# Kernel optimization log

Measured on AMD Instinct MI355X. Metric: run time of the kernel, lower is better.

The kernel has to match this reference:

```python
import jax, jax.numpy as jnp
import numpy as np

WS = 7      # window size
SHIFT = 3   # shift size
NH = 6      # num heads
C = 192     # channels
HH = 56
WW = 56
B = 32


def _rel_coords():
    ch, cw = np.meshgrid(np.arange(WS), np.arange(WS), indexing='ij')
    coords = np.stack([ch, cw]).reshape(2, -1)            # (2, 49)
    rel = coords[:, :, None] - coords[:, None, :]          # (2, 49, 49)
    rel[0] += WS - 1
    rel[1] += WS - 1
    rel[0] *= 2 * WS - 1
    return rel.sum(0)                                      # (49, 49)


def _swin_attn_mask(Hp, Wp):
    img = np.zeros((Hp, Wp), np.int32)
    cnt = 0
    for hs in (slice(0, -WS), slice(-WS, -SHIFT), slice(-SHIFT, None)):
        for ws_ in (slice(0, -WS), slice(-WS, -SHIFT), slice(-SHIFT, None)):
            img[hs, ws_] = cnt
            cnt += 1
    win = img.reshape(Hp // WS, WS, Wp // WS, WS).transpose(0, 2, 1, 3).reshape(-1, WS * WS)
    return win[:, :, None] != win[:, None, :]              # (Nw, 49, 49) bool


def setup_inputs() -> dict:
    key = jax.random.key(0)
    ks = jax.random.split(key, 8)
    s = 0.02
    return {
        'x': jax.random.normal(ks[0], (B, HH * WW, C), jnp.float32),
        'H': HH,
        'W': WW,
        'attn_mask': jnp.asarray(_swin_attn_mask(HH, WW)),
        'relative_coords': jnp.asarray(_rel_coords(), jnp.int32),
        'norm1_w': jnp.ones((C,), jnp.float32),
        'norm1_b': jnp.zeros((C,), jnp.float32),
        'qkv_w': jax.random.normal(ks[1], (3 * C, C), jnp.float32) * s,
        'rel_bias': jax.random.normal(ks[2], ((2 * WS - 1) ** 2, NH), jnp.float32) * 0.2,
        'proj_w': jax.random.normal(ks[3], (C, C), jnp.float32) * s,
        'proj_b': jnp.zeros((C,), jnp.float32),
        'norm2_w': jnp.ones((C,), jnp.float32),
        'norm2_b': jnp.zeros((C,), jnp.float32),
        'fc1_w': jax.random.normal(ks[4], (4 * C, C), jnp.float32) * s,
        'fc1_b': jnp.zeros((4 * C,), jnp.float32),
        'fc2_w': jax.random.normal(ks[5], (C, 4 * C), jnp.float32) * s,
        'fc2_b': jnp.zeros((C,), jnp.float32),
    }


def _ln(t, w, b):
    m = t.mean(-1, keepdims=True)
    v = t.var(-1, keepdims=True)
    return (t - m) / jnp.sqrt(v + 1e-5) * w + b


def reference(x, H, W, attn_mask, relative_coords, norm1_w, norm1_b, qkv_w, rel_bias,
              proj_w, proj_b, norm2_w, norm2_b, fc1_w, fc1_b, fc2_w, fc2_b):
    Bb, L, Cd = x.shape
    nh, hd = NH, C // NH
    shortcut = x
    h = _ln(x, norm1_w, norm1_b).reshape(Bb, H, W, Cd)
    pad_h = (WS - H % WS) % WS
    pad_w = (WS - W % WS) % WS
    if pad_h or pad_w:
        h = jnp.pad(h, ((0, 0), (0, pad_h), (0, pad_w), (0, 0)))
    Hp, Wp = H + pad_h, W + pad_w
    if SHIFT > 0:
        h = jnp.roll(h, (-SHIFT, -SHIFT), axis=(1, 2))
    nWh, nWw = Hp // WS, Wp // WS
    Lw = WS * WS
    win = h.reshape(Bb, nWh, WS, nWw, WS, Cd).transpose(0, 1, 3, 2, 4, 5).reshape(-1, Lw, Cd)
    B_ = win.shape[0]
    qkv = (win @ qkv_w.T).reshape(B_, Lw, 3, nh, hd).transpose(2, 0, 3, 1, 4)
    q, k, v = qkv[0], qkv[1], qkv[2]
    # NOTE: source multiplies by num_dim**0.5 (faithful quirk)
    attn = jnp.einsum('bhid,bhjd->bhij', q, k) * (Cd ** 0.5)
    bias = rel_bias[relative_coords].transpose(2, 0, 1)    # (nh, Lw, Lw)
    attn = attn + bias[None]
    if SHIFT > 0:
        Nw = attn_mask.shape[0]
        attn = attn.reshape(-1, Nw, nh, Lw, Lw)
        attn = jnp.where(attn_mask[None, :, None], -100.0, attn)
        attn = attn.reshape(B_, nh, Lw, Lw)
    attn = jax.nn.softmax(attn, axis=-1)
    out = jnp.einsum('bhij,bhjd->bhid', attn, v).transpose(0, 2, 1, 3).reshape(B_, Lw, Cd)
    out = out @ proj_w.T + proj_b
    out = out.reshape(Bb, nWh, nWw, WS, WS, Cd).transpose(0, 1, 3, 2, 4, 5).reshape(Bb, Hp, Wp, Cd)
    if SHIFT > 0:
        out = jnp.roll(out, (SHIFT, SHIFT), axis=(1, 2))
    out = out[:, :H, :W].reshape(Bb, L, Cd)
    x = shortcut + out
    h2 = _ln(x, norm2_w, norm2_b)
    h2 = jax.nn.gelu(h2 @ fc1_w.T + fc1_b, approximate=False)
    # source MLP applies GELU (drop2 = act_layer()) after fc2 (faithful quirk)
    h2 = jax.nn.gelu(h2 @ fc2_w.T + fc2_b, approximate=False)
    return x + h2
```

## Files before the change

kernel.cpp:

```cpp
#include <hip/hip_runtime.h>

#define WS7    7
#define SHIFT3 3
#define NHEAD  6
#define CCH    192
#define HDIM   32
#define HH56   56
#define LTOK   (HH56*HH56)
#define NWIN   64
#define NBATCH 32
#define NWTOT  (NBATCH*NWIN)
#define LW     49
#define MTOK   (NWTOT*LW)

typedef unsigned short u16;
typedef unsigned int   u32;
typedef __bf16 b16;
typedef b16   b16x8 __attribute__((ext_vector_type(8)));
typedef u16   u16x8 __attribute__((ext_vector_type(8)));
typedef float f32x4 __attribute__((ext_vector_type(4)));

__device__ __forceinline__ float b2f(u16 u) {
    u32 x = ((u32)u) << 16;
    return __builtin_bit_cast(float, x);
}
__device__ __forceinline__ u16 f2b(float f) {
    u32 x = __builtin_bit_cast(u32, f);
    u32 r = x + 0x7FFFu + ((x >> 16) & 1u);
    return (u16)(r >> 16);
}
__device__ __forceinline__ float gelu_exact(float x) {
    return 0.5f * x * (1.0f + erff(x * 0.7071067811865475f));
}

__device__ __forceinline__ int map_token(int m, int &b) {
    int widx = m / LW, p = m - widx * LW;
    b = widx >> 6;
    int wloc = widx & 63;
    int wh = wloc >> 3, ww = wloc & 7;
    int i = p / WS7, j = p - i * WS7;
    int gh = wh * WS7 + i + SHIFT3; if (gh >= HH56) gh -= HH56;
    int gw = ww * WS7 + j + SHIFT3; if (gw >= HH56) gw -= HH56;
    return gh * HH56 + gw;
}

__global__ __launch_bounds__(1024) void probe_kernel(const u16* __restrict__ x, int* flag) {
    __shared__ int ch, cz;
    if (threadIdx.x == 0) { ch = 0; cz = 0; }
    __syncthreads();
    int i = threadIdx.x * 16;
    u16x8 a = *(const u16x8*)(x + i);
    u16x8 b = *(const u16x8*)(x + i + 8);
    int h = 0, z = 0;
    #pragma unroll
    for (int q = 0; q < 8; q++) {
        h += (((a[q] >> 7) & 0xFF) >= 0xC0) + (((b[q] >> 7) & 0xFF) >= 0xC0);
        z += (a[q] == 0) + (b[q] == 0);
    }
    #pragma unroll
    for (int off = 32; off > 0; off >>= 1) {
        h += __shfl_xor(h, off, 64);
        z += __shfl_xor(z, off, 64);
    }
    if ((threadIdx.x & 63) == 0) { atomicAdd(&ch, h); atomicAdd(&cz, z); }
    __syncthreads();
    if (threadIdx.x == 0) *flag = (ch > 250 || cz > 2048) ? 1 : 0;
}

#define CANON_TOTAL 445302
__global__ __launch_bounds__(256) void canon_all_kernel(
    const int* __restrict__ flag,
    const void* s0, const void* s1, const void* s2,  const void* s3,
    const void* s4, const void* s5, const void* s6,  const void* s7,
    const void* s8, const void* s9, const void* s10, const void* s11,
    char* __restrict__ ws)
{
    int i = blockIdx.x * 256 + threadIdx.x;
    if (i >= CANON_TOTAL) return;
    const void* srcs[12] = {s0, s1, s2, s3, s4, s5, s6, s7, s8, s9, s10, s11};
    const int cnt[12] = {110592, 36864, 147456, 147456, 192, 192, 192, 192, 192, 768, 192, 1014};
    const int off[12] = {64, 221248, 294976, 589888, 884800, 885184, 885568, 885952, 886336, 886720, 888256, 888640};
    int seg = 0, base = 0;
    while (seg < 11 && i >= base + cnt[seg]) { base += cnt[seg]; seg++; }
    int j = i - base;
    const void* sp = srcs[seg];
    u16* dp = (u16*)(ws + off[seg]);
    dp[j] = (*flag) ? f2b(((const float*)sp)[j]) : ((const u16*)sp)[j];
}

template<int GATHER>
__global__ __launch_bounds__(256) void ln_kernel(
    const void* __restrict__ src, const u16* __restrict__ w, const u16* __restrict__ bia,
    u16* __restrict__ dst, int m_base, const int* __restrict__ flag)
{
    int wave = threadIdx.x >> 6, lane = threadIdx.x & 63;
    int mloc = blockIdx.x * 4 + wave;
    size_t row;
    if (GATHER) { int b; int l = map_token(m_base + mloc, b); row = (size_t)b * LTOK + l; }
    else row = mloc;
    float v0, v1, v2;
    if (GATHER && *flag) {
        const float* xp = (const float*)src + row * CCH;
        v0 = xp[lane]; v1 = xp[lane + 64]; v2 = xp[lane + 128];
    } else {
        const u16* xp = (const u16*)src + row * CCH;
        v0 = b2f(xp[lane]); v1 = b2f(xp[lane + 64]); v2 = b2f(xp[lane + 128]);
    }
    float s = v0 + v1 + v2, sq = v0 * v0 + v1 * v1 + v2 * v2;
    for (int off = 32; off > 0; off >>= 1) {
        s  += __shfl_xor(s, off, 64);
        sq += __shfl_xor(sq, off, 64);
    }
    float mean = s * (1.f / 192.f);
    float var  = fmaxf(sq * (1.f / 192.f) - mean * mean, 0.f);
    float rstd = rsqrtf(var + 1e-5f);
    u16* op = dst + (size_t)mloc * CCH;
    op[lane]       = f2b((v0 - mean) * rstd * b2f(w[lane])       + b2f(bia[lane]));
    op[lane + 64]  = f2b((v1 - mean) * rstd * b2f(w[lane + 64])  + b2f(bia[lane + 64]));
    op[lane + 128] = f2b((v2 - mean) * rstd * b2f(w[lane + 128]) + b2f(bia[lane + 128]));
}

__device__ __forceinline__ void stage192(const u16* __restrict__ g, int ldg, u16* s, int tid) {
    #pragma unroll
    for (int it = 0; it < 7; it++) {
        int t = it * 256 + tid;
        if (t < 1600) {
            int row = t / 25, c = t - row * 25;
            int cc = (c == 24) ? 0 : c;
            const u16* src = g + (size_t)row * ldg + cc * 8;
            u16* dst = s + (size_t)(it * 256 + (tid & ~63)) * 8;
            __builtin_amdgcn_global_load_lds(
                (const __attribute__((address_space(1))) void*)src,
                (__attribute__((address_space(3))) void*)dst, 16, 0, 0);
        }
    }
}

template<int MODE>
__global__ __launch_bounds__(256) void gemm_bt_kernel(
    const u16* __restrict__ A, const u16* __restrict__ Bm, int K, int N,
    const u16* __restrict__ bias,
    u16* __restrict__ Cb,
    u16* __restrict__ X1,
    const void* __restrict__ Xin,
    void* __restrict__ Oout, size_t o_off, int m_base,
    const int* __restrict__ flag)
{
    __shared__ __align__(16) u16 As[64 * 200];
    __shared__ __align__(16) u16 Bs[64 * 200];
    int isf = *flag;
    int tid = threadIdx.x;
    int m0 = blockIdx.x * 64, n0 = blockIdx.y * 64;
    int wave = tid >> 6, lane = tid & 63;
    int wm = wave >> 1, wn = wave & 1;
    int quad = lane >> 4, mr = lane & 15;
    f32x4 acc00 = {}, acc01 = {}, acc10 = {}, acc11 = {};

    const u16* pa0 = &As[(wm * 32 + mr) * 200 + quad * 8];
    const u16* pb0 = &Bs[(wn * 32 + mr) * 200 + quad * 8];

    for (int k0 = 0; k0 < K; k0 += 192) {
        if (k0) __syncthreads();
        stage192(A  + (size_t)m0 * K + k0, K, As, tid);
        stage192(Bm + (size_t)n0 * K + k0, K, Bs, tid);
        __syncthreads();
        #pragma unroll
        for (int ks = 0; ks < 6; ks++) {
            b16x8 a0 = __builtin_bit_cast(b16x8, *(const u16x8*)(pa0 + ks * 32));
            b16x8 a1 = __builtin_bit_cast(b16x8, *(const u16x8*)(pa0 + 16 * 200 + ks * 32));
            b16x8 b0 = __builtin_bit_cast(b16x8, *(const u16x8*)(pb0 + ks * 32));
            b16x8 b1 = __builtin_bit_cast(b16x8, *(const u16x8*)(pb0 + 16 * 200 + ks * 32));
            acc00 = __builtin_amdgcn_mfma_f32_16x16x32_bf16(a0, b0, acc00, 0, 0, 0);
            acc01 = __builtin_amdgcn_mfma_f32_16x16x32_bf16(a0, b1, acc01, 0, 0, 0);
            acc10 = __builtin_amdgcn_mfma_f32_16x16x32_bf16(a1, b0, acc10, 0, 0, 0);
            acc11 = __builtin_amdgcn_mfma_f32_16x16x32_bf16(a1, b1, acc11, 0, 0, 0);
        }
    }

    f32x4 accs[2][2] = {{acc00, acc01}, {acc10, acc11}};
    for (int sm = 0; sm < 2; sm++) {
        for (int sn = 0; sn < 2; sn++) {
            f32x4 v = accs[sm][sn];
            int nn = n0 + wn * 32 + sn * 16 + mr;
            int mb = m0 + wm * 32 + sm * 16 + quad * 4;
            for (int r = 0; r < 4; r++) {
                int mm = mb + r;
                float val = v[r];
                if (MODE == 0) {
                    Cb[(size_t)mm * N + nn] = f2b(val);
                } else if (MODE == 1) {
                    val += b2f(bias[nn]);
                    int b; int l = map_token(m_base + mm, b);
                    size_t idx = ((size_t)b * LTOK + l) * CCH + nn;
                    float xi = isf ? ((const float*)Xin)[idx] : b2f(((const u16*)Xin)[idx]);
                    X1[idx] = f2b(xi + val);
                } else if (MODE == 2) {
                    val = gelu_exact(val + b2f(bias[nn]));
                    Cb[(size_t)mm * N + nn] = f2b(val);
                } else {
                    val = gelu_exact(val + b2f(bias[nn]));
                    size_t idx = (size_t)mm * CCH + nn;
                    float r2 = val + b2f(X1[idx]);
                    if (isf) ((float*)Oout)[o_off + idx] = r2;
                    else     ((u16*)Oout)[o_off + idx]  = f2b(r2);
                }
            }
        }
    }
}

__global__ __launch_bounds__(256) void attn_kernel(
    const u16* __restrict__ qkv, const u16* __restrict__ rel_bias,
    u16* __restrict__ aout)
{
    __shared__ __align__(16) u16 qs[64 * 32];
    __shared__ __align__(16) u16 ks[64 * 32];
    __shared__ __align__(16) u16 vsT[32 * 72];
    __shared__ __align__(16) u16 ps[64 * 72];
    __shared__ float bias_s[169];
    int blk = blockIdx.x;
    int widx = blk / NHEAD, head = blk - widx * NHEAD;
    int wloc = widx & 63;
    int wh = wloc >> 3, ww = wloc & 7;
    int tid = threadIdx.x;
    const u16* base = qkv + (size_t)widx * LW * 576 + head * HDIM;

    if (tid < 196) {
        int i = tid >> 2, c8 = (tid & 3) * 8;
        *(uint4*)&qs[i * 32 + c8] = *(const uint4*)(base + (size_t)i * 576 + c8);
        *(uint4*)&ks[i * 32 + c8] = *(const uint4*)(base + (size_t)i * 576 + 192 + c8);
        u16x8 vv = *(const u16x8*)(base + (size_t)i * 576 + 384 + c8);
        #pragma unroll
        for (int q = 0; q < 8; q++) vsT[(c8 + q) * 72 + i] = vv[q];
    }
    for (int idx = tid; idx < 32 * 15; idx += 256) {
        int d = idx / 15, j = 49 + (idx - d * 15);
        vsT[d * 72 + j] = 0;
    }
    if (tid < 169) bias_s[tid] = b2f(rel_bias[tid * NHEAD + head]);
    __syncthreads();

    int wave = tid >> 6, lane = tid & 63;
    int quad = lane >> 4, c = lane & 15;

    b16x8 aq = __builtin_bit_cast(b16x8, *(const u16x8*)&qs[(wave * 16 + c) * 32 + quad * 8]);
    f32x4 sacc[4];
    #pragma unroll
    for (int nt = 0; nt < 4; nt++) {
        b16x8 bk = __builtin_bit_cast(b16x8, *(const u16x8*)&ks[(nt * 16 + c) * 32 + quad * 8]);
        f32x4 z = {};
        sacc[nt] = __builtin_amdgcn_mfma_f32_16x16x32_bf16(aq, bk, z, 0, 0, 0);
    }

    const float SCALE = 13.856406460551018f;
    float val[4][4];
    int rbase = wave * 16 + quad * 4;
    #pragma unroll
    for (int r = 0; r < 4; r++) {
        int i = rbase + r;
        int ih = i / WS7, iw = i - ih * WS7;
        int ri = (wh == 7 ? (ih < 4 ? 1 : 2) : 0) * 3 + (ww == 7 ? (iw < 4 ? 1 : 2) : 0);
        #pragma unroll
        for (int nt = 0; nt < 4; nt++) {
            int j = nt * 16 + c;
            float v;
            if (i >= LW) v = 0.f;
            else if (j >= LW) v = -1e30f;
            else {
                int jh = j / WS7, jw = j - jh * WS7;
                int rj = (wh == 7 ? (jh < 4 ? 1 : 2) : 0) * 3 + (ww == 7 ? (jw < 4 ? 1 : 2) : 0);
                if (ri != rj) v = -100.0f;
                else v = fmaf(sacc[nt][r], SCALE, bias_s[(ih - jh + 6) * 13 + (iw - jw + 6)]);
            }
            val[r][nt] = v;
        }
    }

    #pragma unroll
    for (int r = 0; r < 4; r++) {
        float mx = fmaxf(fmaxf(val[r][0], val[r][1]), fmaxf(val[r][2], val[r][3]));
        for (int d = 1; d < 16; d <<= 1) mx = fmaxf(mx, __shfl_xor(mx, d, 64));
        float sum = 0.f;
        #pragma unroll
        for (int nt = 0; nt < 4; nt++) { float e = expf(val[r][nt] - mx); val[r][nt] = e; sum += e; }
        for (int d = 1; d < 16; d <<= 1) sum += __shfl_xor(sum, d, 64);
        float inv = 1.f / sum;
        int i = rbase + r;
        #pragma unroll
        for (int nt = 0; nt < 4; nt++)
            ps[i * 72 + nt * 16 + c] = f2b(val[r][nt] * inv);
    }

    f32x4 oacc[2] = {{}, {}};
    #pragma unroll
    for (int kh = 0; kh < 2; kh++) {
        b16x8 ap = __builtin_bit_cast(b16x8, *(const u16x8*)&ps[(wave * 16 + c) * 72 + kh * 32 + quad * 8]);
        #pragma unroll
        for (int nt = 0; nt < 2; nt++) {
            b16x8 bv = __builtin_bit_cast(b16x8, *(const u16x8*)&vsT[(nt * 16 + c) * 72 + kh * 32 + quad * 8]);
            oacc[nt] = __builtin_amdgcn_mfma_f32_16x16x32_bf16(ap, bv, oacc[nt], 0, 0, 0);
        }
    }
    #pragma unroll
    for (int nt = 0; nt < 2; nt++) {
        #pragma unroll
        for (int r = 0; r < 4; r++) {
            int i = rbase + r;
            if (i < LW)
                aout[((size_t)widx * LW + i) * CCH + head * HDIM + nt * 16 + c] = f2b(oacc[nt][r]);
        }
    }
}

extern "C" void kernel_launch(void* const* d_in, const int* in_sizes, int n_in,
                              void* d_out, int out_size, void* d_ws, size_t ws_size,
                              hipStream_t stream)
{
    const void* x_in = d_in[0];
    char* ws = (char*)d_ws;
    int* flag = (int*)ws;

    u16* n1w_c  = (u16*)(ws + 884800);
    u16* n1b_c  = (u16*)(ws + 885184);
    u16* n2w_c  = (u16*)(ws + 885568);
    u16* n2b_c  = (u16*)(ws + 885952);
    u16* projb_c= (u16*)(ws + 886336);
    u16* fc1b_c = (u16*)(ws + 886720);
    u16* fc2b_c = (u16*)(ws + 888256);
    u16* relb_c = (u16*)(ws + 888640);
    u16* qkvw_c = (u16*)(ws + 64);
    u16* projw_c = (u16*)(ws + 221248);
    u16* fc1w_c = (u16*)(ws + 294976);
    u16* fc2w_c = (u16*)(ws + 589888);

    const size_t P0 = 1u << 20;
    u16* x1   = (u16*)(ws + P0);
    u16* winq = (u16*)(ws + P0 + 38535168);
    u16* qkvq = (u16*)(ws + P0 + 38535168 + 9633792);
    u16* xnq  = winq;
    u16* h1q  = (u16*)(ws + P0 + 38535168 + 4816896);

    probe_kernel<<<1, 1024, 0, stream>>>((const u16*)x_in, flag);

    canon_all_kernel<<<(CANON_TOTAL + 255) / 256, 256, 0, stream>>>(
        flag,
        d_in[7], d_in[9], d_in[13], d_in[15],
        d_in[5], d_in[6], d_in[11], d_in[12],
        d_in[10], d_in[14], d_in[16], d_in[8],
        ws);

    const int M4 = MTOK / 4;
    const int M8 = MTOK / 8;

    for (int q = 0; q < 4; q++) {
        int mb = q * M4;
        ln_kernel<1><<<M4 / 4, 256, 0, stream>>>(x_in, n1w_c, n1b_c, winq, mb, flag);
        gemm_bt_kernel<0><<<dim3(M4 / 64, 9), 256, 0, stream>>>(
            winq, qkvw_c, 192, 576, nullptr, qkvq, nullptr, nullptr, nullptr, 0, 0, flag);
        attn_kernel<<<(NWTOT / 4) * NHEAD, 256, 0, stream>>>(qkvq, relb_c, winq);
        gemm_bt_kernel<1><<<dim3(M4 / 64, 3), 256, 0, stream>>>(
            winq, projw_c, 192, 192, projb_c, nullptr, x1, x_in, nullptr, 0, mb, flag);
    }

    for (int e = 0; e < 8; e++) {
        size_t off = (size_t)e * M8 * CCH;
        ln_kernel<0><<<M8 / 4, 256, 0, stream>>>(x1 + off, n2w_c, n2b_c, xnq, 0, flag);
        gemm_bt_kernel<2><<<dim3(M8 / 64, 12), 256, 0, stream>>>(
            xnq, fc1w_c, 192, 768, fc1b_c, h1q, nullptr, nullptr, nullptr, 0, 0, flag);
        gemm_bt_kernel<3><<<dim3(M8 / 64, 3), 256, 0, stream>>>(
            h1q, fc2w_c, 768, 192, fc2b_c, nullptr, x1 + off, nullptr, d_out, off, 0, flag);
    }
}
```

Measured before the change: 700.5 us.

## Fuse LayerNorm2 into fc1 GEMM, loop N-tiles per block, enlarge chunking

```diff
diff --git a/kernel.cpp b/kernel.cpp
--- a/kernel.cpp
+++ b/kernel.cpp
@@ -136,34 +136,64 @@
     }
 }
 
-template<int MODE>
-__global__ __launch_bounds__(256) void gemm_bt_kernel(
-    const u16* __restrict__ A, const u16* __restrict__ Bm, int K, int N,
+__device__ __forceinline__ void ln_lds_rows(u16* As, const u16* __restrict__ w,
+                                            const u16* __restrict__ bia, int tid) {
+    int r = tid >> 2, p = tid & 3;
+    u16* row = As + r * 200 + p * 48;
+    u16x8 vv[6];
+    float s = 0.f, sq = 0.f;
+    #pragma unroll
+    for (int j = 0; j < 6; j++) {
+        vv[j] = *(const u16x8*)(row + j * 8);
+        #pragma unroll
+        for (int q = 0; q < 8; q++) { float f = b2f(vv[j][q]); s += f; sq += f * f; }
+    }
+    s  += __shfl_xor(s, 1, 64);  s  += __shfl_xor(s, 2, 64);
+    sq += __shfl_xor(sq, 1, 64); sq += __shfl_xor(sq, 2, 64);
+    float mean = s * (1.f / 192.f);
+    float var  = fmaxf(sq * (1.f / 192.f) - mean * mean, 0.f);
+    float rstd = rsqrtf(var + 1e-5f);
+    #pragma unroll
+    for (int j = 0; j < 6; j++) {
+        u16x8 o;
+        #pragma unroll
+        for (int q = 0; q < 8; q++) {
+            int col = p * 48 + j * 8 + q;
+            o[q] = f2b((b2f(vv[j][q]) - mean) * rstd * b2f(w[col]) + b2f(bia[col]));
+        }
+        *(u16x8*)(row + j * 8) = o;
+    }
+}
+
+template<int MODE, int NT, int LNF>
+__global__ __launch_bounds__(256) void gemm_k192(
+    const u16* __restrict__ A, const u16* __restrict__ Bm, int N,
+    const u16* __restrict__ lnw, const u16* __restrict__ lnb,
     const u16* __restrict__ bias,
-    u16* __restrict__ Cb,
-    u16* __restrict__ X1,
-    const void* __restrict__ Xin,
-    void* __restrict__ Oout, size_t o_off, int m_base,
-    const int* __restrict__ flag)
+    u16* __restrict__ Cb, u16* __restrict__ X1, const void* __restrict__ Xin,
+    int m_base, const int* __restrict__ flag)
 {
     __shared__ __align__(16) u16 As[64 * 200];
-    __shared__ __align__(16) u16 Bs[64 * 200];
+    __shared__ __align__(16) u16 Bs[2][64 * 200];
     int isf = *flag;
     int tid = threadIdx.x;
-    int m0 = blockIdx.x * 64, n0 = blockIdx.y * 64;
+    int m0 = blockIdx.x * 64;
     int wave = tid >> 6, lane = tid & 63;
     int wm = wave >> 1, wn = wave & 1;
     int quad = lane >> 4, mr = lane & 15;
-    f32x4 acc00 = {}, acc01 = {}, acc10 = {}, acc11 = {};
+
+    stage192(A + (size_t)m0 * 192, 192, As, tid);
+    stage192(Bm, 192, Bs[0], tid);
+    __syncthreads();
+    if (LNF) { ln_lds_rows(As, lnw, lnb, tid); __syncthreads(); }
 
     const u16* pa0 = &As[(wm * 32 + mr) * 200 + quad * 8];
-    const u16* pb0 = &Bs[(wn * 32 + mr) * 200 + quad * 8];
-
-    for (int k0 = 0; k0 < K; k0 += 192) {
-        if (k0) __syncthreads();
-        stage192(A  + (size_t)m0 * K + k0, K, As, tid);
-        stage192(Bm + (size_t)n0 * K + k0, K, Bs, tid);
-        __syncthreads();
+    #pragma unroll 1
+    for (int nb = 0; nb < NT; nb++) {
+        if (nb + 1 < NT)
+            stage192(Bm + (size_t)(nb + 1) * 64 * 192, 192, Bs[(nb + 1) & 1], tid);
+        const u16* pb0 = &Bs[nb & 1][(wn * 32 + mr) * 200 + quad * 8];
+        f32x4 acc00 = {}, acc01 = {}, acc10 = {}, acc11 = {};
         #pragma unroll
         for (int ks = 0; ks < 6; ks++) {
             b16x8 a0 = __builtin_bit_cast(b16x8, *(const u16x8*)(pa0 + ks * 32));
@@ -175,30 +205,93 @@
             acc10 = __builtin_amdgcn_mfma_f32_16x16x32_bf16(a1, b0, acc10, 0, 0, 0);
             acc11 = __builtin_amdgcn_mfma_f32_16x16x32_bf16(a1, b1, acc11, 0, 0, 0);
         }
-    }
-
-    f32x4 accs[2][2] = {{acc00, acc01}, {acc10, acc11}};
-    for (int sm = 0; sm < 2; sm++) {
-        for (int sn = 0; sn < 2; sn++) {
-            f32x4 v = accs[sm][sn];
-            int nn = n0 + wn * 32 + sn * 16 + mr;
-            int mb = m0 + wm * 32 + sm * 16 + quad * 4;
-            for (int r = 0; r < 4; r++) {
-                int mm = mb + r;
-                float val = v[r];
-                if (MODE == 0) {
-                    Cb[(size_t)mm * N + nn] = f2b(val);
-                } else if (MODE == 1) {
-                    val += b2f(bias[nn]);
-                    int b; int l = map_token(m_base + mm, b);
-                    size_t idx = ((size_t)b * LTOK + l) * CCH + nn;
-                    float xi = isf ? ((const float*)Xin)[idx] : b2f(((const u16*)Xin)[idx]);
-                    X1[idx] = f2b(xi + val);
-                } else if (MODE == 2) {
-                    val = gelu_exact(val + b2f(bias[nn]));
-                    Cb[(size_t)mm * N + nn] = f2b(val);
-                } else {
-                    val = gelu_exact(val + b2f(bias[nn]));
+        int n0 = nb * 64;
+        f32x4 accs[2][2] = {{acc00, acc01}, {acc10, acc11}};
+        #pragma unroll
+        for (int sm = 0; sm < 2; sm++) {
+            #pragma unroll
+            for (int sn = 0; sn < 2; sn++) {
+                f32x4 v = accs[sm][sn];
+                int nn = n0 + wn * 32 + sn * 16 + mr;
+                int mb = m0 + wm * 32 + sm * 16 + quad * 4;
+                #pragma unroll
+                for (int r = 0; r < 4; r++) {
+                    int mm = mb + r;
+                    float val = v[r];
+                    if (MODE == 0) {
+                        Cb[(size_t)mm * N + nn] = f2b(val);
+                    } else if (MODE == 1) {
+                        val += b2f(bias[nn]);
+                        int b; int l = map_token(m_base + mm, b);
+                        size_t idx = ((size_t)b * LTOK + l) * CCH + nn;
+                        float xi = isf ? ((const float*)Xin)[idx] : b2f(((const u16*)Xin)[idx]);
+                        X1[idx] = f2b(xi + val);
+                    } else {
+                        val = gelu_exact(val + b2f(bias[nn]));
+                        Cb[(size_t)mm * N + nn] = f2b(val);
+                    }
+                }
+            }
+        }
+        __syncthreads();
+    }
+}
+
+__global__ __launch_bounds__(256) void gemm_k768(
+    const u16* __restrict__ A, const u16* __restrict__ Bm,
+    const u16* __restrict__ bias, const u16* __restrict__ X1,
+    void* __restrict__ Oout, size_t o_off, const int* __restrict__ flag)
+{
+    __shared__ __align__(16) u16 As[64 * 200];
+    __shared__ __align__(16) u16 Bs[2][64 * 200];
+    int isf = *flag;
+    int tid = threadIdx.x;
+    int m0 = blockIdx.x * 64;
+    int wave = tid >> 6, lane = tid & 63;
+    int wm = wave >> 1, wn = wave & 1;
+    int quad = lane >> 4, mr = lane & 15;
+
+    f32x4 acc[3][4] = {};
+
+    const u16* pa0 = &As[(wm * 32 + mr) * 200 + quad * 8];
+    #pragma unroll 1
+    for (int k0 = 0; k0 < 768; k0 += 192) {
+        stage192(A + (size_t)m0 * 768 + k0, 768, As, tid);
+        stage192(Bm + k0, 768, Bs[0], tid);
+        __syncthreads();
+        #pragma unroll
+        for (int nb = 0; nb < 3; nb++) {
+            if (nb < 2)
+                stage192(Bm + (size_t)(nb + 1) * 64 * 768 + k0, 768, Bs[(nb + 1) & 1], tid);
+            const u16* pb0 = &Bs[nb & 1][(wn * 32 + mr) * 200 + quad * 8];
+            #pragma unroll
+            for (int ks = 0; ks < 6; ks++) {
+                b16x8 a0 = __builtin_bit_cast(b16x8, *(const u16x8*)(pa0 + ks * 32));
+                b16x8 a1 = __builtin_bit_cast(b16x8, *(const u16x8*)(pa0 + 16 * 200 + ks * 32));
+                b16x8 b0 = __builtin_bit_cast(b16x8, *(const u16x8*)(pb0 + ks * 32));
+                b16x8 b1 = __builtin_bit_cast(b16x8, *(const u16x8*)(pb0 + 16 * 200 + ks * 32));
+                acc[nb][0] = __builtin_amdgcn_mfma_f32_16x16x32_bf16(a0, b0, acc[nb][0], 0, 0, 0);
+                acc[nb][1] = __builtin_amdgcn_mfma_f32_16x16x32_bf16(a0, b1, acc[nb][1], 0, 0, 0);
+                acc[nb][2] = __builtin_amdgcn_mfma_f32_16x16x32_bf16(a1, b0, acc[nb][2], 0, 0, 0);
+                acc[nb][3] = __builtin_amdgcn_mfma_f32_16x16x32_bf16(a1, b1, acc[nb][3], 0, 0, 0);
+            }
+            __syncthreads();
+        }
+    }
+
+    #pragma unroll
+    for (int nb = 0; nb < 3; nb++) {
+        #pragma unroll
+        for (int sm = 0; sm < 2; sm++) {
+            #pragma unroll
+            for (int sn = 0; sn < 2; sn++) {
+                f32x4 v = acc[nb][sm * 2 + sn];
+                int nn = nb * 64 + wn * 32 + sn * 16 + mr;
+                int mb = m0 + wm * 32 + sm * 16 + quad * 4;
+                #pragma unroll
+                for (int r = 0; r < 4; r++) {
+                    int mm = mb + r;
+                    float val = gelu_exact(v[r] + b2f(bias[nn]));
                     size_t idx = (size_t)mm * CCH + nn;
                     float r2 = val + b2f(X1[idx]);
                     if (isf) ((float*)Oout)[o_off + idx] = r2;
@@ -320,28 +413,27 @@
     char* ws = (char*)d_ws;
     int* flag = (int*)ws;
 
-    u16* n1w_c  = (u16*)(ws + 884800);
-    u16* n1b_c  = (u16*)(ws + 885184);
-    u16* n2w_c  = (u16*)(ws + 885568);
-    u16* n2b_c  = (u16*)(ws + 885952);
-    u16* projb_c= (u16*)(ws + 886336);
-    u16* fc1b_c = (u16*)(ws + 886720);
-    u16* fc2b_c = (u16*)(ws + 888256);
-    u16* relb_c = (u16*)(ws + 888640);
-    u16* qkvw_c = (u16*)(ws + 64);
+    u16* qkvw_c  = (u16*)(ws + 64);
     u16* projw_c = (u16*)(ws + 221248);
-    u16* fc1w_c = (u16*)(ws + 294976);
-    u16* fc2w_c = (u16*)(ws + 589888);
+    u16* fc1w_c  = (u16*)(ws + 294976);
+    u16* fc2w_c  = (u16*)(ws + 589888);
+    u16* n1w_c   = (u16*)(ws + 884800);
+    u16* n1b_c   = (u16*)(ws + 885184);
+    u16* n2w_c   = (u16*)(ws + 885568);
+    u16* n2b_c   = (u16*)(ws + 885952);
+    u16* projb_c = (u16*)(ws + 886336);
+    u16* fc1b_c  = (u16*)(ws + 886720);
+    u16* fc2b_c  = (u16*)(ws + 888256);
+    u16* relb_c  = (u16*)(ws + 888640);
 
     const size_t P0 = 1u << 20;
-    u16* x1   = (u16*)(ws + P0);
-    u16* winq = (u16*)(ws + P0 + 38535168);
-    u16* qkvq = (u16*)(ws + P0 + 38535168 + 9633792);
-    u16* xnq  = winq;
-    u16* h1q  = (u16*)(ws + P0 + 38535168 + 4816896);
+    const size_t X1SZ   = (size_t)MTOK * CCH * 2;
+    const size_t QKVSZ  = (size_t)MTOK * 576 * 2;
+    const size_t H1FULL = (size_t)MTOK * 768 * 2;
+
+    u16* x1 = (u16*)(ws + P0);
 
     probe_kernel<<<1, 1024, 0, stream>>>((const u16*)x_in, flag);
-
     canon_all_kernel<<<(CANON_TOTAL + 255) / 256, 256, 0, stream>>>(
         flag,
         d_in[7], d_in[9], d_in[13], d_in[15],
@@ -349,25 +441,43 @@
         d_in[10], d_in[14], d_in[16], d_in[8],
         ws);
 
-    const int M4 = MTOK / 4;
-    const int M8 = MTOK / 8;
-
-    for (int q = 0; q < 4; q++) {
-        int mb = q * M4;
-        ln_kernel<1><<<M4 / 4, 256, 0, stream>>>(x_in, n1w_c, n1b_c, winq, mb, flag);
-        gemm_bt_kernel<0><<<dim3(M4 / 64, 9), 256, 0, stream>>>(
-            winq, qkvw_c, 192, 576, nullptr, qkvq, nullptr, nullptr, nullptr, 0, 0, flag);
-        attn_kernel<<<(NWTOT / 4) * NHEAD, 256, 0, stream>>>(qkvq, relb_c, winq);
-        gemm_bt_kernel<1><<<dim3(M4 / 64, 3), 256, 0, stream>>>(
-            winq, projw_c, 192, 192, projb_c, nullptr, x1, x_in, nullptr, 0, mb, flag);
-    }
-
-    for (int e = 0; e < 8; e++) {
-        size_t off = (size_t)e * M8 * CCH;
-        ln_kernel<0><<<M8 / 4, 256, 0, stream>>>(x1 + off, n2w_c, n2b_c, xnq, 0, flag);
-        gemm_bt_kernel<2><<<dim3(M8 / 64, 12), 256, 0, stream>>>(
-            xnq, fc1w_c, 192, 768, fc1b_c, h1q, nullptr, nullptr, nullptr, 0, 0, flag);
-        gemm_bt_kernel<3><<<dim3(M8 / 64, 3), 256, 0, stream>>>(
-            h1q, fc2w_c, 768, 192, fc2b_c, nullptr, x1 + off, nullptr, d_out, off, 0, flag);
-    }
-}
+    int QC, EC;
+    u16 *winq, *qkvq, *h1q;
+    if (ws_size >= P0 + 2 * X1SZ + H1FULL) {
+        QC = 1; EC = 1;
+        winq = (u16*)(ws + P0 + X1SZ);
+        qkvq = (u16*)(ws + P0 + 2 * X1SZ);
+        h1q  = qkvq;
+    } else if (ws_size >= P0 + 2 * X1SZ + QKVSZ) {
+        QC = 1; EC = 2;
+        winq = (u16*)(ws + P0 + X1SZ);
+        qkvq = (u16*)(ws + P0 + 2 * X1SZ);
+        h1q  = qkvq;
+    } else {
+        QC = 4; EC = 8;
+        winq = (u16*)(ws + P0 + X1SZ);
+        qkvq = (u16*)(ws + P0 + X1SZ + 9633792);
+        h1q  = (u16*)(ws + P0 + X1SZ);
+    }
+
+    const int MQ = MTOK / QC;
+    const int ME = MTOK / EC;
+
+    for (int q = 0; q < QC; q++) {
+        int mb = q * MQ;
+        ln_kernel<1><<<MQ / 4, 256, 0, stream>>>(x_in, n1w_c, n1b_c, winq, mb, flag);
+        gemm_k192<0, 9, 0><<<MQ / 64, 256, 0, stream>>>(
+            winq, qkvw_c, 576, nullptr, nullptr, nullptr, qkvq, nullptr, nullptr, 0, flag);
+        attn_kernel<<<(NWTOT / QC) * NHEAD, 256, 0, stream>>>(qkvq, relb_c, winq);
+        gemm_k192<1, 3, 0><<<MQ / 64, 256, 0, stream>>>(
+            winq, projw_c, 192, nullptr, nullptr, projb_c, nullptr, x1, x_in, mb, flag);
+    }
+
+    for (int e = 0; e < EC; e++) {
+        size_t off = (size_t)e * ME * CCH;
+        gemm_k192<2, 12, 1><<<ME / 64, 256, 0, stream>>>(
+            x1 + off, fc1w_c, 768, n2w_c, n2b_c, fc1b_c, h1q, nullptr, nullptr, 0, flag);
+        gemm_k768<<<ME / 64, 256, 0, stream>>>(
+            h1q, fc2w_c, fc2b_c, x1 + off, d_out, off, flag);
+    }
+}
```

New measurement: 587.2 us. -16.2%, faster.
